# Performance work log

Hardware: AMD Instinct MI355X
Metric: run time of the kernel (lower is better)

Reference implementation:

```python
import jax, jax.numpy as jnp
import numpy as np

N_LAYERS = 4
N_WIRES = 10


def _apply_1q(state, U, wire, n):
    # state: [B, 2^n] complex64; U: [2,2] or [B,2,2]
    B = state.shape[0]
    a, b = 2 ** wire, 2 ** (n - wire - 1)
    s = state.reshape(B, a, 2, b)
    if U.ndim == 2:
        s = jnp.einsum('ij,bxjy->bxiy', U, s)
    else:
        s = jnp.einsum('bij,bxjy->bxiy', U, s)
    return s.reshape(B, -1)


def _apply_cnot(state, c, t, n):
    # CNOT with control c, target t (wire 0 = most significant bit, PennyLane convention)
    B = state.shape[0]
    q1, q2 = min(c, t), max(c, t)
    d1, d2, d3 = 2 ** q1, 2 ** (q2 - q1 - 1), 2 ** (n - q2 - 1)
    s = state.reshape(B, d1, 2, d2, 2, d3)
    if c < t:
        # control on axis 2, flip (X) target axis 4 where control bit == 1
        s = jnp.concatenate([s[:, :, 0:1], jnp.flip(s[:, :, 1:2], axis=4)], axis=2)
    else:
        # control on axis 4, flip target axis 2 where control bit == 1
        s = jnp.concatenate([s[:, :, :, :, 0:1], jnp.flip(s[:, :, :, :, 1:2], axis=2)], axis=4)
    return s.reshape(B, -1)


def _ry_mat(theta):
    # theta: [B] -> [B,2,2] complex64
    c, s = jnp.cos(theta / 2), jnp.sin(theta / 2)
    return jnp.stack([jnp.stack([c, -s], -1), jnp.stack([s, c], -1)], -2).astype(jnp.complex64)


def _rot_mat(phi, theta, omega):
    # qml.Rot(phi, theta, omega) = RZ(omega) @ RY(theta) @ RZ(phi)
    e = lambda a: jnp.exp(1j * a.astype(jnp.complex64))
    c = jnp.cos(theta / 2).astype(jnp.complex64)
    s = jnp.sin(theta / 2).astype(jnp.complex64)
    m00 = e(-0.5 * (phi + omega)) * c
    m01 = -e(0.5 * (phi - omega)) * s
    m10 = e(-0.5 * (phi - omega)) * s
    m11 = e(0.5 * (phi + omega)) * c
    return jnp.stack([jnp.stack([m00, m01]), jnp.stack([m10, m11])])


def setup_inputs() -> dict:
    key = jax.random.key(0)
    kx, kw = jax.random.split(key)
    X = jax.random.uniform(kx, (16384, N_WIRES), dtype=jnp.float32)
    # weightsStrongly = pi * U(0,1) of shape (n_layers, n_wires, 3)
    weights = np.pi * jax.random.uniform(kw, (N_LAYERS, N_WIRES, 3), dtype=jnp.float32)
    bias = jnp.zeros((1,), dtype=jnp.float32)
    return {"X": X, "weights": weights, "bias": bias}


def reference(X, weights, bias):
    B, n = X.shape
    L = weights.shape[0]
    # |0...0> batched statevector
    state = jnp.zeros((B, 2 ** n), dtype=jnp.complex64).at[:, 0].set(1.0)
    # angle encoding, gates='Y': RY(x_i * pi/2) on wire i (per-sample angle)
    for w in range(n):
        state = _apply_1q(state, _ry_mat(X[:, w] * (np.pi / 2)), w, n)
    # StronglyEntanglingLayers: Rot on each wire, then ring of CNOTs with range r_l
    for l in range(L):
        for w in range(n):
            U = _rot_mat(weights[l, w, 0], weights[l, w, 1], weights[l, w, 2])
            state = _apply_1q(state, U, w, n)
        r = l % (n - 1) + 1
        for w in range(n):
            state = _apply_cnot(state, w, (w + r) % n, n)
    # numClasses=2 -> single measurement: expval(PauliZ(wire n-1)) (last wire = LSB)
    probs = (state.real ** 2 + state.imag ** 2).reshape(B, 2 ** (n - 1), 2)
    z = jnp.sum(probs[..., 0] - probs[..., 1], axis=-1)  # [B]
    return z[:, None] + bias[None, :]  # [B, 1]
```

## Files before the change

### kernel.cpp

```cpp
#include <hip/hip_runtime.h>
#include <cstdint>
#include <utility>

#define NW 10
#define NL 4


typedef float v2 __attribute__((ext_vector_type(2)));
typedef unsigned int u32x2 __attribute__((ext_vector_type(2)));

#if defined(__has_builtin)
#if __has_builtin(__builtin_amdgcn_permlane16_swap) && __has_builtin(__builtin_amdgcn_permlane32_swap)
#define HAVE_PERMLANE_SWAP 1
#endif
#endif

struct Plan {
    int n;
    uint16_t pmask[40];
    uint16_t rmask[40];
    uint8_t  lw[40];
    uint16_t measmask;
};

constexpr bool keep_rot(int l, int w) {
    if (l <= 1) return true;
    if (l == 2) return w != 7;
    return w == 1 || w == 5 || w == 9;
}

constexpr Plan make_plan() {
    Plan P{};
    unsigned row[10], cI[10];
    for (int b = 0; b < 10; ++b) { row[b] = 1u << b; cI[b] = 1u << b; }
    P.n = 0;
    for (int l = 0; l < NL; ++l) {
        for (int w = 0; w < NW; ++w) {
            if (l > 0 && keep_rot(l, w)) {
                const int b = 9 - w;
                P.pmask[P.n] = (uint16_t)cI[b];
                P.rmask[P.n] = (uint16_t)row[b];
                P.lw[P.n]    = (uint8_t)(l * NW + w);
                P.n++;
            }
        }
        const int r = l % (NW - 1) + 1;
        for (int w = 0; w < NW; ++w) {
            const int cb = 9 - w, tb = 9 - ((w + r) % NW);
            row[tb] ^= row[cb];
            cI[cb]  ^= cI[tb];
        }
    }
    P.measmask = (uint16_t)row[0];
    return P;
}

constexpr Plan PL = make_plan();
constexpr int NROT = 22;
static_assert(PL.n == NROT, "plan size mismatch");

template<int MASK>
__device__ __forceinline__ float swz(float v, int lane) {
    if constexpr (MASK == 1) {
        return __int_as_float(__builtin_amdgcn_mov_dpp(__float_as_int(v), 0xB1, 0xF, 0xF, true));
    } else if constexpr (MASK == 2) {
        return __int_as_float(__builtin_amdgcn_mov_dpp(__float_as_int(v), 0x4E, 0xF, 0xF, true));
    } else if constexpr (MASK == 3) {
        return __int_as_float(__builtin_amdgcn_mov_dpp(__float_as_int(v), 0x1B, 0xF, 0xF, true));
    } else if constexpr (MASK == 7) {
        return __int_as_float(__builtin_amdgcn_mov_dpp(__float_as_int(v), 0x141, 0xF, 0xF, true));
    } else if constexpr (MASK == 15) {
        return __int_as_float(__builtin_amdgcn_mov_dpp(__float_as_int(v), 0x140, 0xF, 0xF, true));
    }
#ifdef HAVE_PERMLANE_SWAP
    else if constexpr (MASK == 16) {
        const u32x2 r = __builtin_amdgcn_permlane16_swap(__float_as_uint(v), __float_as_uint(v), false, false);
        return __uint_as_float((lane & 16) ? r.x : r.y);
    } else if constexpr (MASK == 32) {
        const u32x2 r = __builtin_amdgcn_permlane32_swap(__float_as_uint(v), __float_as_uint(v), false, false);
        return __uint_as_float((lane & 32) ? r.x : r.y);
    } else if constexpr (MASK == 48) {
        const u32x2 r = __builtin_amdgcn_permlane32_swap(__float_as_uint(v), __float_as_uint(v), false, false);
        const unsigned t = (lane & 32) ? r.x : r.y;
        const u32x2 r2 = __builtin_amdgcn_permlane16_swap(t, t, false, false);
        return __uint_as_float((lane & 16) ? r2.x : r2.y);
    }
#endif
    else if constexpr (MASK < 32) {
        return __int_as_float(__builtin_amdgcn_ds_swizzle(
            __float_as_int(v), (MASK << 10) | 0x1F));
    } else {
        return __int_as_float(__builtin_amdgcn_ds_bpermute(
            (lane << 2) ^ (MASK << 2), __float_as_int(v)));
    }
}

template<int MASK>
__device__ __forceinline__ v2 swz2(v2 v, int lane) {
    v2 r;
    r.x = swz<MASK>(v.x, lane);
    r.y = swz<MASK>(v.y, lane);
    return r;
}

__device__ __forceinline__ v2 mkv2(float a, float b) { v2 r; r.x = a; r.y = b; return r; }

__device__ __forceinline__ void cmul2(v2 ar, v2 ai, v2 br, v2 bi, v2& cr, v2& ci) {
    cr = ar * br - ai * bi;
    ci = ar * bi + ai * br;
}

__device__ __forceinline__ void upd(v2& xr, v2& xi, v2 pr, v2 pi,
                                    float cmr, float coi, float bmi, float bor,
                                    bool S) {
    const float emi = S ? -bmi : bmi;
    const float eor = S ? -bor : bor;
    const v2 nr = cmr * xr - emi * xi + eor * pr - coi * pi;
    const v2 ni = cmr * xi + emi * xr + eor * pi + coi * pr;
    xr = nr; xi = ni;
}

template<int G>
__device__ __forceinline__ void apply_rot(v2 (&sr)[16], v2 (&si)[16],
                                          const float4* __restrict__ rotm,
                                          int lane) {
    constexpr unsigned pm = PL.pmask[G], rm = PL.rmask[G];
    constexpr int pLoc = pm & 15, pLane = (int)(pm >> 4);
    constexpr int rLoc = rm & 15, rLane = (int)(rm >> 4);
    const float4 m = rotm[PL.lw[G]];
    const bool rl = (__popc(lane & rLane) & 1) != 0;
    const float cmr = m.x, coi = m.w;
    const float bmi = rl ? -m.y : m.y;
    const float bor = rl ? -m.z : m.z;

    if constexpr (pLane == 0) {
#pragma unroll
        for (int j = 0; j < 16; ++j) {
            const int k = j ^ pLoc;
            if (j < k) {
                const v2 ajr = sr[j], aji = si[j];
                const v2 akr = sr[k], aki = si[k];
                upd(sr[j], si[j], akr, aki, cmr, coi, bmi, bor,
                    (__builtin_popcount(j & rLoc) & 1) != 0);
                upd(sr[k], si[k], ajr, aji, cmr, coi, bmi, bor,
                    (__builtin_popcount(k & rLoc) & 1) != 0);
            }
        }
    } else if constexpr (pLoc == 0) {
#pragma unroll
        for (int j = 0; j < 16; ++j) {
            const v2 pr = swz2<pLane>(sr[j], lane);
            const v2 pi = swz2<pLane>(si[j], lane);
            upd(sr[j], si[j], pr, pi, cmr, coi, bmi, bor,
                (__builtin_popcount(j & rLoc) & 1) != 0);
            if (j == 7 || j == 15) __builtin_amdgcn_sched_barrier(0);
        }
    } else {
#pragma unroll
        for (int j = 0; j < 16; ++j) {
            const int k = j ^ pLoc;
            if (j < k) {
                const v2 pjr = swz2<pLane>(sr[k], lane);
                const v2 pji = swz2<pLane>(si[k], lane);
                const v2 pkr = swz2<pLane>(sr[j], lane);
                const v2 pki = swz2<pLane>(si[j], lane);
                upd(sr[j], si[j], pjr, pji, cmr, coi, bmi, bor,
                    (__builtin_popcount(j & rLoc) & 1) != 0);
                upd(sr[k], si[k], pkr, pki, cmr, coi, bmi, bor,
                    (__builtin_popcount(k & rLoc) & 1) != 0);
            }
            if (j == 7 || j == 15) __builtin_amdgcn_sched_barrier(0);
        }
    }
}

template<int... Gs>
__device__ __forceinline__ void apply_all(v2 (&sr)[16], v2 (&si)[16],
                                          const float4* __restrict__ rotm,
                                          int lane,
                                          std::integer_sequence<int, Gs...>) {
    (apply_rot<Gs>(sr, si, rotm, lane), ...);
}

__global__ __launch_bounds__(256, 4) void vqc_kernel(const float* __restrict__ X,
                                                     const float* __restrict__ W,
                                                     const float* __restrict__ bias,
                                                     float* __restrict__ out,
                                                     int n_pairs) {
    __shared__ float4 rotm[NL * NW];
    const int t = threadIdx.x;

    if (t < NL * NW) {
        const float phi = W[t * 3 + 0], th = W[t * 3 + 1], om = W[t * 3 + 2];
        float sh, ch; sincosf(0.5f * th, &sh, &ch);
        float s0, c0; sincosf(-0.5f * (phi + om), &s0, &c0);
        float s1, c1; sincosf( 0.5f * (phi - om), &s1, &c1);
        rotm[t] = make_float4(c0 * ch, s0 * ch, -c1 * sh, -s1 * sh);
    }
    __syncthreads();

    const int wave = (blockIdx.x * blockDim.x + t) >> 6;
    const int lane = t & 63;
    if (wave >= n_pairs) return;

    const float* xp = X + (size_t)(2 * wave) * NW;

    v2 hr, hi;
#pragma unroll
    for (int w = 0; w < 6; ++w) {
        float s0, c0, s1, c1;
        __sincosf(xp[w]      * 0.78539816339744831f, &s0, &c0);
        __sincosf(xp[w + NW] * 0.78539816339744831f, &s1, &c1);
        const v2 s = mkv2(s0, s1), c = mkv2(c0, c1);
        const float4 m = rotm[w];
        const v2 a0r = m.x * c + m.z * s;
        const v2 a0i = m.y * c + m.w * s;
        const v2 a1r = m.x * s - m.z * c;
        const v2 a1i = m.w * c - m.y * s;
        const bool b = (lane >> (5 - w)) & 1;
        const v2 br = b ? a1r : a0r;
        const v2 bi = b ? a1i : a0i;
        if (w == 0) { hr = br; hi = bi; }
        else {
            v2 nr, ni; cmul2(hr, hi, br, bi, nr, ni);
            hr = nr; hi = ni;
        }
    }
    v2 t0r[4], t0i[4], t1r[4], t1i[4];
#pragma unroll
    for (int w = 6; w < 10; ++w) {
        float s0, c0, s1, c1;
        __sincosf(xp[w]      * 0.78539816339744831f, &s0, &c0);
        __sincosf(xp[w + NW] * 0.78539816339744831f, &s1, &c1);
        const v2 s = mkv2(s0, s1), c = mkv2(c0, c1);
        const float4 m = rotm[w];
        t0r[w - 6] = m.x * c + m.z * s;
        t0i[w - 6] = m.y * c + m.w * s;
        t1r[w - 6] = m.x * s - m.z * c;
        t1i[w - 6] = m.w * c - m.y * s;
    }
    v2 Ar[4], Ai[4], Br[4], Bi[4];
#pragma unroll
    for (int u = 0; u < 4; ++u) {
        const int hb = (u >> 1) & 1, lb = u & 1;
        cmul2(hb ? t1r[0] : t0r[0], hb ? t1i[0] : t0i[0],
              lb ? t1r[1] : t0r[1], lb ? t1i[1] : t0i[1], Ar[u], Ai[u]);
        cmul2(hb ? t1r[2] : t0r[2], hb ? t1i[2] : t0i[2],
              lb ? t1r[3] : t0r[3], lb ? t1i[3] : t0i[3], Br[u], Bi[u]);
    }
    v2 HAr[4], HAi[4];
#pragma unroll
    for (int u = 0; u < 4; ++u) cmul2(hr, hi, Ar[u], Ai[u], HAr[u], HAi[u]);

    v2 sr[16], si[16];
#pragma unroll
    for (int j = 0; j < 16; ++j) {
        cmul2(HAr[j >> 2], HAi[j >> 2], Br[j & 3], Bi[j & 3], sr[j], si[j]);
    }

    apply_all(sr, si, rotm, lane, std::make_integer_sequence<int, NROT>{});

    constexpr unsigned mm = PL.measmask;
    constexpr int mLoc = mm & 15, mLane = (int)(mm >> 4);
    v2 acc = mkv2(0.0f, 0.0f);
#pragma unroll
    for (int j = 0; j < 16; ++j) {
        const v2 p = sr[j] * sr[j] + si[j] * si[j];
        if (__builtin_popcount(j & mLoc) & 1) acc -= p; else acc += p;
    }
    if (__popc(lane & mLane) & 1) acc = -acc;
    acc += swz2<1>(acc, lane);
    acc += swz2<2>(acc, lane);
    acc += swz2<4>(acc, lane);
    acc += swz2<8>(acc, lane);
    acc += swz2<16>(acc, lane);
    acc += swz2<32>(acc, lane);
    if (lane == 0) {
        const float b0 = bias[0];
        out[2 * wave]     = acc.x + b0;
        out[2 * wave + 1] = acc.y + b0;
    }
}

extern "C" void kernel_launch(void* const* d_in, const int* in_sizes, int n_in,
                              void* d_out, int out_size, void* d_ws, size_t ws_size,
                              hipStream_t stream) {
    const float* X    = (const float*)d_in[0];
    const float* W    = (const float*)d_in[1];
    const float* bias = (const float*)d_in[2];
    float* out = (float*)d_out;
    const int n_samples = in_sizes[0] / NW;
    const int n_pairs = n_samples / 2;
    const int threads = 256;
    const int blocks = (n_pairs * 64 + threads - 1) / threads;
    hipLaunchKernelGGL(vqc_kernel, dim3(blocks), dim3(threads), 0, stream,
                       X, W, bias, out, n_pairs);
}
```

Baseline: 138.4 us.

## Remap state index basis with GF(2) transform to reduce cross-lane shuffle cost

Adds a compile-time linear change of basis over GF(2) (TMAT and its inverse) that relabels which state-index bits live in lanes versus register slots. Rotation pair and phase masks and the measurement mask are remapped to match, and the initial product-state lane selection becomes a parity over a lane mask. The intent is to give the rotations cheaper lane partner masks, such as DPP-friendly ones, so the permlane-swap path can be dropped. It also removes the sched_barrier hints and relaxes launch bounds from 4 to 2 waves per EU, which gives the compiler more registers at the cost of occupancy.

New measurement: 126.8 us. 8.4% less time.

```diff
diff --git a/kernel.cpp b/kernel.cpp
--- a/kernel.cpp
+++ b/kernel.cpp
@@ -7,13 +7,50 @@
 
 
 typedef float v2 __attribute__((ext_vector_type(2)));
-typedef unsigned int u32x2 __attribute__((ext_vector_type(2)));
-
-#if defined(__has_builtin)
-#if __has_builtin(__builtin_amdgcn_permlane16_swap) && __has_builtin(__builtin_amdgcn_permlane32_swap)
-#define HAVE_PERMLANE_SWAP 1
-#endif
-#endif
+
+struct Cols10 { unsigned c[10]; };
+struct Rows10 { unsigned r[10]; };
+
+constexpr Cols10 TMAT = {{
+    0x001, 0x002, 0x004, 0x008,
+    0x070, 0x080, 0x100, 0x130, 0x210, 0x200
+}};
+
+constexpr unsigned tmap(unsigned m) {
+    unsigned r = 0;
+    for (int b = 0; b < 10; ++b) if ((m >> b) & 1u) r ^= TMAT.c[b];
+    return r;
+}
+
+constexpr Rows10 invertT() {
+    unsigned a[10] = {}, inv[10] = {};
+    for (int i = 0; i < 10; ++i) {
+        for (int j = 0; j < 10; ++j) a[i] |= ((TMAT.c[j] >> i) & 1u) << j;
+        inv[i] = 1u << i;
+    }
+    for (int col = 0; col < 10; ++col) {
+        int piv = -1;
+        for (int r2 = col; r2 < 10; ++r2) if ((a[r2] >> col) & 1u) { piv = r2; break; }
+        unsigned ta = a[piv]; a[piv] = a[col]; a[col] = ta;
+        unsigned ti = inv[piv]; inv[piv] = inv[col]; inv[col] = ti;
+        for (int r2 = 0; r2 < 10; ++r2)
+            if (r2 != col && ((a[r2] >> col) & 1u)) { a[r2] ^= a[col]; inv[r2] ^= inv[col]; }
+    }
+    Rows10 R{};
+    for (int i = 0; i < 10; ++i) R.r[i] = inv[i];
+    return R;
+}
+constexpr Rows10 RROW = invertT();
+
+constexpr unsigned rmap(unsigned rowmask) {
+    unsigned r = 0;
+    for (int b = 0; b < 10; ++b) if ((rowmask >> b) & 1u) r ^= RROW.r[b];
+    return r;
+}
+
+static_assert(RROW.r[0] == 1 && RROW.r[1] == 2 && RROW.r[2] == 4 && RROW.r[3] == 8, "slot rows");
+static_assert((RROW.r[4] & 15) == 0 && (RROW.r[5] & 15) == 0 && (RROW.r[6] & 15) == 0 &&
+              (RROW.r[7] & 15) == 0 && (RROW.r[8] & 15) == 0 && (RROW.r[9] & 15) == 0, "lane rows");
 
 struct Plan {
     int n;
@@ -38,8 +75,8 @@
         for (int w = 0; w < NW; ++w) {
             if (l > 0 && keep_rot(l, w)) {
                 const int b = 9 - w;
-                P.pmask[P.n] = (uint16_t)cI[b];
-                P.rmask[P.n] = (uint16_t)row[b];
+                P.pmask[P.n] = (uint16_t)tmap(cI[b]);
+                P.rmask[P.n] = (uint16_t)rmap(row[b]);
                 P.lw[P.n]    = (uint8_t)(l * NW + w);
                 P.n++;
             }
@@ -51,13 +88,18 @@
             cI[cb]  ^= cI[tb];
         }
     }
-    P.measmask = (uint16_t)row[0];
+    P.measmask = (uint16_t)rmap(row[0]);
     return P;
 }
 
 constexpr Plan PL = make_plan();
 constexpr int NROT = 22;
 static_assert(PL.n == NROT, "plan size mismatch");
+
+constexpr int LSEL[6] = {
+    (int)(RROW.r[9] >> 4), (int)(RROW.r[8] >> 4), (int)(RROW.r[7] >> 4),
+    (int)(RROW.r[6] >> 4), (int)(RROW.r[5] >> 4), (int)(RROW.r[4] >> 4)
+};
 
 template<int MASK>
 __device__ __forceinline__ float swz(float v, int lane) {
@@ -71,22 +113,7 @@
         return __int_as_float(__builtin_amdgcn_mov_dpp(__float_as_int(v), 0x141, 0xF, 0xF, true));
     } else if constexpr (MASK == 15) {
         return __int_as_float(__builtin_amdgcn_mov_dpp(__float_as_int(v), 0x140, 0xF, 0xF, true));
-    }
-#ifdef HAVE_PERMLANE_SWAP
-    else if constexpr (MASK == 16) {
-        const u32x2 r = __builtin_amdgcn_permlane16_swap(__float_as_uint(v), __float_as_uint(v), false, false);
-        return __uint_as_float((lane & 16) ? r.x : r.y);
-    } else if constexpr (MASK == 32) {
-        const u32x2 r = __builtin_amdgcn_permlane32_swap(__float_as_uint(v), __float_as_uint(v), false, false);
-        return __uint_as_float((lane & 32) ? r.x : r.y);
-    } else if constexpr (MASK == 48) {
-        const u32x2 r = __builtin_amdgcn_permlane32_swap(__float_as_uint(v), __float_as_uint(v), false, false);
-        const unsigned t = (lane & 32) ? r.x : r.y;
-        const u32x2 r2 = __builtin_amdgcn_permlane16_swap(t, t, false, false);
-        return __uint_as_float((lane & 16) ? r2.x : r2.y);
-    }
-#endif
-    else if constexpr (MASK < 32) {
+    } else if constexpr (MASK < 32) {
         return __int_as_float(__builtin_amdgcn_ds_swizzle(
             __float_as_int(v), (MASK << 10) | 0x1F));
     } else {
@@ -153,7 +180,6 @@
             const v2 pi = swz2<pLane>(si[j], lane);
             upd(sr[j], si[j], pr, pi, cmr, coi, bmi, bor,
                 (__builtin_popcount(j & rLoc) & 1) != 0);
-            if (j == 7 || j == 15) __builtin_amdgcn_sched_barrier(0);
         }
     } else {
 #pragma unroll
@@ -169,7 +195,6 @@
                 upd(sr[k], si[k], pkr, pki, cmr, coi, bmi, bor,
                     (__builtin_popcount(k & rLoc) & 1) != 0);
             }
-            if (j == 7 || j == 15) __builtin_amdgcn_sched_barrier(0);
         }
     }
 }
@@ -182,7 +207,7 @@
     (apply_rot<Gs>(sr, si, rotm, lane), ...);
 }
 
-__global__ __launch_bounds__(256, 4) void vqc_kernel(const float* __restrict__ X,
+__global__ __launch_bounds__(256, 2) void vqc_kernel(const float* __restrict__ X,
                                                      const float* __restrict__ W,
                                                      const float* __restrict__ bias,
                                                      float* __restrict__ out,
@@ -217,7 +242,7 @@
         const v2 a0i = m.y * c + m.w * s;
         const v2 a1r = m.x * s - m.z * c;
         const v2 a1i = m.w * c - m.y * s;
-        const bool b = (lane >> (5 - w)) & 1;
+        const bool b = (__popc(lane & LSEL[w]) & 1) != 0;
         const v2 br = b ? a1r : a0r;
         const v2 bi = b ? a1i : a0i;
         if (w == 0) { hr = br; hi = bi; }
```
